# Kernel optimization log

Measured on AMD Instinct MI355X. Metric: run time of the kernel, lower is better.

The kernel has to match this reference:

```python
import jax, jax.numpy as jnp
import numpy as np

BS, DIM, EMB_DIM, SRC, TDEC, NEMB = 64, 512, 512, 400, 100, 50257


def intra_attention(h_t, h, W_attn):
    # h_t: [bs, dim]; h: [n, bs, dim]; W_attn: [dim, dim]
    n, bs, dim = h.shape
    # Faithful to torch .view([bs, dim, n]) on a contiguous [n, bs, dim]
    # tensor: raw row-major memory reinterpretation (NOT a transpose).
    hv = jnp.reshape(h, (bs, dim, n))  # [bs, dim, n]
    # E_t = (h_t @ W) [bs,1,dim] bmm hv [bs,dim,n] -> [bs, n]
    E = jnp.einsum('bd,bdn->bn', h_t @ W_attn, hv)
    # sum-normalized (non-softmax) score, eq. (4)
    A = E / jnp.sum(E, axis=1, keepdims=True)  # [bs, n]
    C = jnp.einsum('bdn,bn->bd', hv, A)        # [bs, dim]
    return A, C


def pointer_generator(ae_t, ce_t, hd_t, cd_t, W_emb, W_proj, W_u, b_u, b_out):
    # c_cat: [3*dim, bs]
    c_cat = jnp.concatenate((hd_t, ce_t, cd_t), axis=1).T
    # p_switch: [bs]
    p_switch = jax.nn.sigmoid(W_u @ c_cat + b_u).squeeze(0)
    # shared-embedding output projection, sect 2.4
    W_out = jnp.tanh(W_emb @ W_proj)           # [n_emb, 3*dim]
    logits = W_out @ c_cat + b_out             # [n_emb, bs]
    p_vocab = jax.nn.softmax(logits, axis=0)   # softmax over vocab
    p_gen = ((1.0 - p_switch) * p_vocab).T     # [bs, n_emb]
    p_copy = p_switch[:, None] * ae_t          # [bs, src]
    return p_gen, p_copy


def setup_inputs() -> dict:
    key = jax.random.key(0)
    ks = jax.random.split(key, 12)
    inp = {
        'h_t': jax.random.uniform(ks[0], (BS, DIM), dtype=jnp.float32),
        'h_enc': jax.random.uniform(ks[1], (SRC, BS, DIM), dtype=jnp.float32),
        'h_dec': jax.random.uniform(ks[2], (TDEC, BS, DIM), dtype=jnp.float32),
        'x': jax.random.randint(ks[3], (SRC, BS, 1), 0, NEMB, dtype=jnp.int64) if jax.config.jax_enable_x64 else jax.random.randint(ks[3], (SRC, BS, 1), 0, NEMB, dtype=jnp.int32),
        # positive attention weights keep the sum-normalized score well-conditioned
        'W_attn_enc': jax.random.uniform(ks[4], (DIM, DIM), dtype=jnp.float32, maxval=0.05),
        'W_attn_dec': jax.random.uniform(ks[5], (DIM, DIM), dtype=jnp.float32, maxval=0.05),
        'W_emb': jax.random.normal(ks[6], (NEMB, EMB_DIM), dtype=jnp.float32) * 0.02,
        'W_proj': jax.random.normal(ks[7], (EMB_DIM, 3 * DIM), dtype=jnp.float32) * 0.02,
        'W_u': jax.random.normal(ks[8], (1, 3 * DIM), dtype=jnp.float32) * 0.02,
        'b_u': jnp.zeros((1,), dtype=jnp.float32),
        'b_out': jnp.zeros((NEMB, 1), dtype=jnp.float32),
    }
    return inp


def reference(h_t, h_enc, h_dec, x, W_attn_enc, W_attn_dec, W_emb, W_proj, W_u, b_u, b_out):
    # one decode step of ReinforcedDecoder: enc attn + dec attn + pointer-gen
    ae_t, ce_t = intra_attention(h_t, h_enc, W_attn_enc)
    ad_t, cd_t = intra_attention(h_t, h_dec, W_attn_dec)
    p_gen, p_copy = pointer_generator(ae_t, ce_t, h_t, cd_t,
                                      W_emb, W_proj, W_u, b_u, b_out)
    return p_gen, p_copy
```

## Files before the change

### kernel.cpp

```cpp
#include <hip/hip_runtime.h>
#include <math.h>

typedef __attribute__((ext_vector_type(8))) short bf16x8;
typedef __attribute__((ext_vector_type(4))) float f32x4;
typedef __attribute__((ext_vector_type(4))) float f4v;

#define BS   64
#define DIM  512
#define SRC  400
#define TDEC 100
#define NEMB 50257
#define K3   1536

#define WS_Q     0
#define WS_EENC  65536
#define WS_EDEC  91136
#define WS_CENC  97536
#define WS_CDEC  130304
#define WS_ESUM  163072
#define WS_PSW   163200
#define WS_SMAX  163264
#define WS_SSUM  163328
#define WS_WPT   163392
#define WS_CCB   556608
#define WS_ZBEG  WS_CENC
#define WS_ZCNT  (WS_WPT - WS_CENC)

__device__ __forceinline__ ushort f2bf(float x) {
    union { float f; unsigned u; } v; v.f = x;
    unsigned r = (v.u + 0x7FFFu + ((v.u >> 16) & 1u)) >> 16;
    return (ushort)r;
}
__device__ __forceinline__ bf16x8 pack8v(f4v a, f4v b) {
    union { ushort us[8]; bf16x8 v; } p;
    p.us[0] = f2bf(a.x); p.us[1] = f2bf(a.y); p.us[2] = f2bf(a.z); p.us[3] = f2bf(a.w);
    p.us[4] = f2bf(b.x); p.us[5] = f2bf(b.y); p.us[6] = f2bf(b.z); p.us[7] = f2bf(b.w);
    return p.v;
}
__device__ __forceinline__ float pade_tanh(float x) {
    const float x2 = x * x;
    const float num = x * fmaf(x2, 1.0f / 15.0f, 1.0f);
    const float den = fmaf(x2, 0.4f, 1.0f);
    return num * __frcp_rn(den);
}
__device__ __forceinline__ void gl2lds16(const void* g, void* l) {
    __builtin_amdgcn_global_load_lds(
        (const __attribute__((address_space(1))) unsigned int*)g,
        (__attribute__((address_space(3))) unsigned int*)l, 16, 0, 0);
}

__global__ __launch_bounds__(256) void k_prep(const float* __restrict__ h_t,
                                              const float* __restrict__ Wenc,
                                              const float* __restrict__ Wdec,
                                              const float* __restrict__ Wp,
                                              float* __restrict__ ws) {
    __shared__ float sh[128 * 68];
    const int tid = threadIdx.x;
    if (blockIdx.x < 32) {
        const int which = blockIdx.x >> 4;
        const int c0 = (blockIdx.x & 15) * 32;
        const float* W = which ? Wdec : Wenc;
        float* q = ws + WS_Q + which * (BS * DIM);
        float* hS = sh;
        float* WSm = sh + 64 * 65;
        const int c = tid & 31, bg = tid >> 5;
        float acc[8] = {0.f, 0.f, 0.f, 0.f, 0.f, 0.f, 0.f, 0.f};
        for (int kc = 0; kc < 8; ++kc) {
            __syncthreads();
            #pragma unroll
            for (int r = 0; r < 16; ++r) {
                const int idx = r * 256 + tid;
                const int b = idx >> 6, k = idx & 63;
                hS[b * 65 + k] = h_t[b * DIM + kc * 64 + k];
            }
            #pragma unroll
            for (int r = 0; r < 8; ++r) {
                const int idx = r * 256 + tid;
                const int k = idx >> 5, cc = idx & 31;
                WSm[k * 33 + cc] = W[(size_t)(kc * 64 + k) * DIM + c0 + cc];
            }
            __syncthreads();
            #pragma unroll 8
            for (int k = 0; k < 64; ++k) {
                const float wv = WSm[k * 33 + c];
                #pragma unroll
                for (int bb = 0; bb < 8; ++bb)
                    acc[bb] = fmaf(hS[(bg * 8 + bb) * 65 + k], wv, acc[bb]);
            }
        }
        #pragma unroll
        for (int bb = 0; bb < 8; ++bb)
            q[(bg * 8 + bb) * DIM + c0 + c] = acc[bb];
    } else {
        const int bid = blockIdx.x - 32;
        const int t = bid >> 2, c = bid & 3;
        float (*T32)[68] = (float (*)[68])sh;
        #pragma unroll
        for (int p = 0; p < 8; ++p) {
            const int idx = p * 256 + tid;
            const int kk = idx >> 4, s = idx & 15;
            const float4 v = *(const float4*)(Wp + (size_t)(c * 128 + kk) * K3 + t * 64 + s * 4);
            T32[kk][s * 4 + 0] = v.x; T32[kk][s * 4 + 1] = v.y;
            T32[kk][s * 4 + 2] = v.z; T32[kk][s * 4 + 3] = v.w;
        }
        __syncthreads();
        char* dst = (char*)(ws + WS_WPT) + (size_t)bid * 16384;
        #pragma unroll
        for (int p = 0; p < 4; ++p) {
            const int fid = p * 256 + tid;
            const int lane = fid & 63;
            const int J = (fid >> 6) & 3;
            const int ks = fid >> 8;
            const int j = J * 16 + (lane & 15);
            const int k0 = ks * 32 + (lane >> 4) * 8;
            f4v a, b;
            a.x = T32[k0 + 0][j]; a.y = T32[k0 + 1][j];
            a.z = T32[k0 + 2][j]; a.w = T32[k0 + 3][j];
            b.x = T32[k0 + 4][j]; b.y = T32[k0 + 5][j];
            b.z = T32[k0 + 6][j]; b.w = T32[k0 + 7][j];
            *(bf16x8*)(dst + fid * 16) = pack8v(a, b);
        }
    }
}

#define IC 16
__global__ __launch_bounds__(256) void k_attn(const float* __restrict__ h_enc,
                                              const float* __restrict__ h_dec,
                                              float* __restrict__ ws) {
    const int b = blockIdx.x, which = blockIdx.y, z = blockIdx.z;
    const int tid = threadIdx.x;
    const int n   = which ? TDEC : SRC;
    const int per = which ? (TDEC / 4) : (SRC / 4);
    const int i_begin = z * per, i_end = i_begin + per;
    const float* h  = which ? h_dec : h_enc;
    const float* q  = ws + WS_Q + which * (BS * DIM) + b * DIM;
    float* wsE      = ws + (which ? WS_EDEC : WS_EENC) + b * n;
    float* Cws      = ws + (which ? WS_CDEC : WS_CENC) + b * DIM;
    const float* hb = h + (size_t)b * DIM * n;

    __shared__ float hS[DIM * (IC + 1)];
    __shared__ float qs[DIM];
    __shared__ float Ered[256];
    __shared__ float Es[IC];

    qs[tid] = q[tid];
    qs[tid + 256] = q[tid + 256];

    const int ii = tid & (IC - 1);
    const int dg = tid >> 4;
    float c0 = 0.f, c1 = 0.f, esum = 0.f;

    for (int i0 = i_begin; i0 < i_end; i0 += IC) {
        const int ic = min(IC, i_end - i0);
        __syncthreads();
        #pragma unroll 8
        for (int idx = tid; idx < DIM * IC; idx += 256) {
            const int d = idx >> 4, i = idx & (IC - 1);
            hS[d * (IC + 1) + i] = (i < ic) ? hb[(size_t)d * n + i0 + i] : 0.f;
        }
        __syncthreads();
        float p = 0.f;
        #pragma unroll 8
        for (int d = dg * 32; d < dg * 32 + 32; ++d) p += qs[d] * hS[d * (IC + 1) + ii];
        Ered[dg * IC + ii] = p;
        __syncthreads();
        if (tid < IC) {
            float e = 0.f;
            #pragma unroll
            for (int g = 0; g < 16; ++g) e += Ered[g * IC + tid];
            Es[tid] = e;
            esum += e;
            if (tid < ic) wsE[i0 + tid] = e;
        }
        __syncthreads();
        #pragma unroll
        for (int i = 0; i < IC; ++i) {
            const float e = Es[i];
            c0 += hS[tid * (IC + 1) + i] * e;
            c1 += hS[(tid + 256) * (IC + 1) + i] * e;
        }
    }
    atomicAdd(&Cws[tid], c0);
    atomicAdd(&Cws[tid + 256], c1);
    __syncthreads();
    if (tid < IC) Ered[tid] = esum;
    __syncthreads();
    if (tid == 0) {
        float s = 0.f;
        #pragma unroll
        for (int g = 0; g < IC; ++g) s += Ered[g];
        atomicAdd(&ws[WS_ESUM + which * 64 + b], s);
    }
}

__global__ void k_pswitch(const float* __restrict__ h_t,
                          const float* __restrict__ W_u,
                          const float* __restrict__ b_u,
                          float* __restrict__ out_copy,
                          float* __restrict__ ws) {
    const int b = blockIdx.x, tid = threadIdx.x;
    const float invE = 1.f / ws[WS_ESUM + b];
    const float invD = 1.f / ws[WS_ESUM + 64 + b];
    const float* Ce = ws + WS_CENC + b * DIM;
    const float* Cd = ws + WS_CDEC + b * DIM;
    ushort* ccB = (ushort*)(ws + WS_CCB);
    __shared__ float red[256];
    float part = 0.f;
    #pragma unroll
    for (int r = 0; r < 6; ++r) {
        const int j = tid + r * 256;
        float v = (j < DIM) ? h_t[b * DIM + j]
                            : ((j < 2 * DIM) ? Ce[j - DIM] * invE : Cd[j - 2 * DIM] * invD);
        ccB[(size_t)b * K3 + j] = f2bf(v);
        part += W_u[j] * v;
    }
    red[tid] = part;
    __syncthreads();
    for (int s = 128; s > 0; s >>= 1) {
        if (tid < s) red[tid] += red[tid + s];
        __syncthreads();
    }
    const float ps = 1.f / (1.f + expf(-(red[0] + b_u[0])));
    if (tid == 0) ws[WS_PSW + b] = ps;
    const float* Ee = ws + WS_EENC + b * SRC;
    for (int i = tid; i < SRC; i += 256) out_copy[b * SRC + i] = ps * Ee[i] * invE;
}

#define VB 128
#define WAITV(N) asm volatile("s_waitcnt vmcnt(" #N ")" ::: "memory")
__global__ __launch_bounds__(256, 2) void k_bigmm(const float* __restrict__ We,
                                                  const float* __restrict__ ws,
                                                  const float* __restrict__ b_out,
                                                  float* __restrict__ out) {
    __shared__ __align__(16) char smem[65536];
    const ushort* ccB = (const ushort*)(ws + WS_CCB);
    const char* wptb  = (const char*)(ws + WS_WPT);

    const int tid  = threadIdx.x;
    const int w    = tid >> 6, lane = tid & 63;
    const int lrow = lane & 15, lgrp = lane >> 4;
    const int vw   = blockIdx.x * VB + w * 32;
    const int row0 = vw + lrow, row1 = vw + 16 + lrow;
    char* tbase = smem + 49152 + w * 4096;
    const int swz = (lrow & 7) << 4;

    #pragma unroll
    for (int p = 0; p < 3; ++p) {
        const char* src = wptb + (size_t)p * 16384 + tid * 16;
        char* dst = smem + p * 16384 + tid * 16;
        #pragma unroll
        for (int rnd = 0; rnd < 4; ++rnd) gl2lds16(src + rnd * 4096, dst + rnd * 4096);
    }

    bf16x8 A0[16], A1[16];
    if (row0 < NEMB) {
        const f4v* p = (const f4v*)(We + (size_t)row0 * DIM + lgrp * 8);
        #pragma unroll
        for (int f = 0; f < 16; ++f)
            A0[f] = pack8v(__builtin_nontemporal_load(p + f * 8),
                           __builtin_nontemporal_load(p + f * 8 + 1));
    } else {
        #pragma unroll
        for (int f = 0; f < 16; ++f) A0[f] = (bf16x8){0, 0, 0, 0, 0, 0, 0, 0};
    }
    if (row1 < NEMB) {
        const f4v* p = (const f4v*)(We + (size_t)row1 * DIM + lgrp * 8);
        #pragma unroll
        for (int f = 0; f < 16; ++f)
            A1[f] = pack8v(__builtin_nontemporal_load(p + f * 8),
                           __builtin_nontemporal_load(p + f * 8 + 1));
    } else {
        #pragma unroll
        for (int f = 0; f < 16; ++f) A1[f] = (bf16x8){0, 0, 0, 0, 0, 0, 0, 0};
    }

    f32x4 La0[4], La1[4], Ta0[4], Ta1[4];
    #pragma unroll
    for (int i = 0; i < 4; ++i) {
        La0[i] = (f32x4){0.f, 0.f, 0.f, 0.f}; La1[i] = (f32x4){0.f, 0.f, 0.f, 0.f};
        Ta0[i] = (f32x4){0.f, 0.f, 0.f, 0.f}; Ta1[i] = (f32x4){0.f, 0.f, 0.f, 0.f};
    }

    for (int it = 0; it < 8; ++it) {
        #pragma unroll
        for (int u = 0; u < 12; ++u) {
            const int i = it * 12 + u;
            if (u == 10)      { if (it == 7) WAITV(4); else WAITV(8); }
            else if (u == 11) { if (it == 7) WAITV(0); else WAITV(8); }
            else              { WAITV(8); }
            __builtin_amdgcn_s_barrier();
            {
                const char* bp = smem + (u % 3) * 16384 + lane * 16;
                #pragma unroll
                for (int ks = 0; ks < 4; ++ks) {
                    const bf16x8 b0 = *(const bf16x8*)(bp + ks * 4096);
                    const bf16x8 b1 = *(const bf16x8*)(bp + ks * 4096 + 1024);
                    const bf16x8 b2 = *(const bf16x8*)(bp + ks * 4096 + 2048);
                    const bf16x8 b3 = *(const bf16x8*)(bp + ks * 4096 + 3072);
                    Ta0[0] = __builtin_amdgcn_mfma_f32_16x16x32_bf16(A0[(u & 3) * 4 + ks], b0, Ta0[0], 0, 0, 0);
                    Ta1[0] = __builtin_amdgcn_mfma_f32_16x16x32_bf16(A1[(u & 3) * 4 + ks], b0, Ta1[0], 0, 0, 0);
                    Ta0[1] = __builtin_amdgcn_mfma_f32_16x16x32_bf16(A0[(u & 3) * 4 + ks], b1, Ta0[1], 0, 0, 0);
                    Ta1[1] = __builtin_amdgcn_mfma_f32_16x16x32_bf16(A1[(u & 3) * 4 + ks], b1, Ta1[1], 0, 0, 0);
                    Ta0[2] = __builtin_amdgcn_mfma_f32_16x16x32_bf16(A0[(u & 3) * 4 + ks], b2, Ta0[2], 0, 0, 0);
                    Ta1[2] = __builtin_amdgcn_mfma_f32_16x16x32_bf16(A1[(u & 3) * 4 + ks], b2, Ta1[2], 0, 0, 0);
                    Ta0[3] = __builtin_amdgcn_mfma_f32_16x16x32_bf16(A0[(u & 3) * 4 + ks], b3, Ta0[3], 0, 0, 0);
                    Ta1[3] = __builtin_amdgcn_mfma_f32_16x16x32_bf16(A1[(u & 3) * 4 + ks], b3, Ta1[3], 0, 0, 0);
                }
            }
            if ((u & 3) == 3) {
                const int t = it * 3 + (u >> 2);
                #pragma unroll
                for (int nj = 0; nj < 4; ++nj) {
                    const int j = nj * 16 + lrow;
                    #pragma unroll
                    for (int r = 0; r < 4; ++r) {
                        const int v = lgrp * 4 + r;
                        *(ushort*)(tbase + v * 128 + ((j * 2) ^ ((v & 7) << 4))) =
                            f2bf(pade_tanh(Ta0[nj][r]));
                        *(ushort*)(tbase + (16 + v) * 128 + ((j * 2) ^ ((v & 7) << 4))) =
                            f2bf(pade_tanh(Ta1[nj][r]));
                    }
                }
                #pragma unroll
                for (int kc = 0; kc < 2; ++kc) {
                    const bf16x8 tf0 = *(const bf16x8*)(tbase + lrow * 128 +
                                                        ((kc * 64 + lgrp * 16) ^ swz));
                    const bf16x8 tf1 = *(const bf16x8*)(tbase + (16 + lrow) * 128 +
                                                        ((kc * 64 + lgrp * 16) ^ swz));
                    const ushort* cc = ccB + (size_t)lrow * K3 + t * 64 + kc * 32 + lgrp * 8;
                    const bf16x8 c0 = *(const bf16x8*)(cc);
                    const bf16x8 c1 = *(const bf16x8*)(cc + 16 * K3);
                    const bf16x8 c2 = *(const bf16x8*)(cc + 32 * K3);
                    const bf16x8 c3 = *(const bf16x8*)(cc + 48 * K3);
                    La0[0] = __builtin_amdgcn_mfma_f32_16x16x32_bf16(tf0, c0, La0[0], 0, 0, 0);
                    La1[0] = __builtin_amdgcn_mfma_f32_16x16x32_bf16(tf1, c0, La1[0], 0, 0, 0);
                    La0[1] = __builtin_amdgcn_mfma_f32_16x16x32_bf16(tf0, c1, La0[1], 0, 0, 0);
                    La1[1] = __builtin_amdgcn_mfma_f32_16x16x32_bf16(tf1, c1, La1[1], 0, 0, 0);
                    La0[2] = __builtin_amdgcn_mfma_f32_16x16x32_bf16(tf0, c2, La0[2], 0, 0, 0);
                    La1[2] = __builtin_amdgcn_mfma_f32_16x16x32_bf16(tf1, c2, La1[2], 0, 0, 0);
                    La0[3] = __builtin_amdgcn_mfma_f32_16x16x32_bf16(tf0, c3, La0[3], 0, 0, 0);
                    La1[3] = __builtin_amdgcn_mfma_f32_16x16x32_bf16(tf1, c3, La1[3], 0, 0, 0);
                }
                #pragma unroll
                for (int z = 0; z < 4; ++z) {
                    Ta0[z] = (f32x4){0.f, 0.f, 0.f, 0.f};
                    Ta1[z] = (f32x4){0.f, 0.f, 0.f, 0.f};
                }
            }
            __builtin_amdgcn_s_barrier();
            if (i + 3 < 96) {
                const char* src = wptb + (size_t)(i + 3) * 16384 + tid * 16;
                char* dst = smem + (u % 3) * 16384 + tid * 16;
                #pragma unroll
                for (int rnd = 0; rnd < 4; ++rnd)
                    gl2lds16(src + rnd * 4096, dst + rnd * 4096);
            }
        }
    }

    #pragma unroll
    for (int nb = 0; nb < 4; ++nb) {
        const int b = nb * 16 + lrow;
        #pragma unroll
        for (int r = 0; r < 4; ++r) {
            const int v0 = vw + lgrp * 4 + r;
            const int v1 = v0 + 16;
            if (v0 < NEMB) out[(size_t)b * NEMB + v0] = La0[nb][r] + b_out[v0];
            if (v1 < NEMB) out[(size_t)b * NEMB + v1] = La1[nb][r] + b_out[v1];
        }
    }
}

__global__ __launch_bounds__(1024) void k_softmax(float* __restrict__ out,
                                                  const float* __restrict__ ws) {
    const int b = blockIdx.x, tid = threadIdx.x;
    float* L = out + (size_t)b * NEMB;
    __shared__ float red[1024];
    float m = -1e30f;
    for (int v = tid; v < NEMB; v += 1024) m = fmaxf(m, L[v]);
    red[tid] = m;
    __syncthreads();
    for (int s = 512; s > 0; s >>= 1) {
        if (tid < s) red[tid] = fmaxf(red[tid], red[tid + s]);
        __syncthreads();
    }
    const float mb = red[0];
    __syncthreads();
    float sum = 0.f;
    for (int v = tid; v < NEMB; v += 1024) sum += expf(L[v] - mb);
    red[tid] = sum;
    __syncthreads();
    for (int s = 512; s > 0; s >>= 1) {
        if (tid < s) red[tid] += red[tid + s];
        __syncthreads();
    }
    const float scale = (1.f - ws[WS_PSW + b]) / red[0];
    for (int v = tid; v < NEMB; v += 1024) L[v] = expf(L[v] - mb) * scale;
}

extern "C" void kernel_launch(void* const* d_in, const int* in_sizes, int n_in,
                              void* d_out, int out_size, void* d_ws, size_t ws_size,
                              hipStream_t stream) {
    const float* h_t        = (const float*)d_in[0];
    const float* h_enc      = (const float*)d_in[1];
    const float* h_dec      = (const float*)d_in[2];
    const float* W_attn_enc = (const float*)d_in[4];
    const float* W_attn_dec = (const float*)d_in[5];
    const float* W_emb      = (const float*)d_in[6];
    const float* W_proj     = (const float*)d_in[7];
    const float* W_u        = (const float*)d_in[8];
    const float* b_u        = (const float*)d_in[9];
    const float* b_out      = (const float*)d_in[10];

    float* out = (float*)d_out;
    float* ws  = (float*)d_ws;
    float* out_copy = out + (size_t)BS * NEMB;

    hipMemsetAsync(ws + WS_ZBEG, 0, (size_t)WS_ZCNT * sizeof(float), stream);
    k_prep   <<<128, 256, 0, stream>>>(h_t, W_attn_enc, W_attn_dec, W_proj, ws);
    k_attn   <<<dim3(64, 2, 4), 256, 0, stream>>>(h_enc, h_dec, ws);
    k_pswitch<<<64, 256, 0, stream>>>(h_t, W_u, b_u, out_copy, ws);
    k_bigmm  <<<(NEMB + VB - 1) / VB, 256, 0, stream>>>(W_emb, ws, b_out, out);
    k_softmax<<<64, 1024, 0, stream>>>(out, ws);
}
```

Measured before the change: 339.0 us.

## Stage context in LDS, double-buffer Wproj, add setprio, split softmax across blocks

The concatenated context vector is now written pre-swizzled into an MFMA fragment layout and streamed into LDS per tile, replacing strided global loads inside the second GEMM. The Wproj pipeline drops from triple to double buffering, which frees LDS for the context tile, and the waitcnt schedule is adjusted to match. MFMA sections are wrapped in s_setprio. The 64-block softmax is replaced by a two-pass split: per-chunk max/sum statistics followed by a wider normalize kernel, to raise parallelism. The trade-off is an extra launch and a shallower prefetch depth.

```diff
diff --git a/kernel.cpp b/kernel.cpp
--- a/kernel.cpp
+++ b/kernel.cpp
@@ -20,9 +20,9 @@
 #define WS_ESUM  163072
 #define WS_PSW   163200
 #define WS_SMAX  163264
-#define WS_SSUM  163328
-#define WS_WPT   163392
-#define WS_CCB   556608
+#define WS_SSUM  163520
+#define WS_WPT   163776
+#define WS_CCF   556992
 #define WS_ZBEG  WS_CENC
 #define WS_ZCNT  (WS_WPT - WS_CENC)
 
@@ -203,15 +203,18 @@
     const float invD = 1.f / ws[WS_ESUM + 64 + b];
     const float* Ce = ws + WS_CENC + b * DIM;
     const float* Cd = ws + WS_CDEC + b * DIM;
-    ushort* ccB = (ushort*)(ws + WS_CCB);
+    ushort* ccF = (ushort*)(ws + WS_CCF);
     __shared__ float red[256];
+    const int nb = b >> 4, bl = b & 15;
     float part = 0.f;
     #pragma unroll
     for (int r = 0; r < 6; ++r) {
         const int j = tid + r * 256;
         float v = (j < DIM) ? h_t[b * DIM + j]
                             : ((j < 2 * DIM) ? Ce[j - DIM] * invE : Cd[j - 2 * DIM] * invD);
-        ccB[(size_t)b * K3 + j] = f2bf(v);
+        const int t = j >> 6, jj = j & 63;
+        const int kc = jj >> 5, lsub = (jj >> 3) & 3, e = jj & 7;
+        ccF[t * 4096 + kc * 2048 + nb * 512 + (lsub * 16 + bl) * 8 + e] = f2bf(v);
         part += W_u[j] * v;
     }
     red[tid] = part;
@@ -232,20 +235,21 @@
                                                   const float* __restrict__ ws,
                                                   const float* __restrict__ b_out,
                                                   float* __restrict__ out) {
-    __shared__ __align__(16) char smem[65536];
-    const ushort* ccB = (const ushort*)(ws + WS_CCB);
-    const char* wptb  = (const char*)(ws + WS_WPT);
+    __shared__ __align__(16) char smem[57344];
+    const char* wptb = (const char*)(ws + WS_WPT);
+    const char* ccfb = (const char*)(ws + WS_CCF);
 
     const int tid  = threadIdx.x;
     const int w    = tid >> 6, lane = tid & 63;
     const int lrow = lane & 15, lgrp = lane >> 4;
     const int vw   = blockIdx.x * VB + w * 32;
     const int row0 = vw + lrow, row1 = vw + 16 + lrow;
-    char* tbase = smem + 49152 + w * 4096;
+    char* ccL   = smem + 32768;
+    char* tbase = smem + 40960 + w * 4096;
     const int swz = (lrow & 7) << 4;
 
     #pragma unroll
-    for (int p = 0; p < 3; ++p) {
+    for (int p = 0; p < 2; ++p) {
         const char* src = wptb + (size_t)p * 16384 + tid * 16;
         char* dst = smem + p * 16384 + tid * 16;
         #pragma unroll
@@ -285,12 +289,13 @@
         #pragma unroll
         for (int u = 0; u < 12; ++u) {
             const int i = it * 12 + u;
-            if (u == 10)      { if (it == 7) WAITV(4); else WAITV(8); }
-            else if (u == 11) { if (it == 7) WAITV(0); else WAITV(8); }
-            else              { WAITV(8); }
+            if (u == 11)           { if (it == 7) { WAITV(0); } else { WAITV(4); } }
+            else if ((u & 3) == 1) { WAITV(6); }
+            else                   { WAITV(4); }
             __builtin_amdgcn_s_barrier();
             {
-                const char* bp = smem + (u % 3) * 16384 + lane * 16;
+                const char* bp = smem + (u & 1) * 16384 + lane * 16;
+                __builtin_amdgcn_s_setprio(1);
                 #pragma unroll
                 for (int ks = 0; ks < 4; ++ks) {
                     const bf16x8 b0 = *(const bf16x8*)(bp + ks * 4096);
@@ -306,9 +311,9 @@
                     Ta0[3] = __builtin_amdgcn_mfma_f32_16x16x32_bf16(A0[(u & 3) * 4 + ks], b3, Ta0[3], 0, 0, 0);
                     Ta1[3] = __builtin_amdgcn_mfma_f32_16x16x32_bf16(A1[(u & 3) * 4 + ks], b3, Ta1[3], 0, 0, 0);
                 }
+                __builtin_amdgcn_s_setprio(0);
             }
             if ((u & 3) == 3) {
-                const int t = it * 3 + (u >> 2);
                 #pragma unroll
                 for (int nj = 0; nj < 4; ++nj) {
                     const int j = nj * 16 + lrow;
@@ -321,17 +326,18 @@
                             f2bf(pade_tanh(Ta1[nj][r]));
                     }
                 }
+                __builtin_amdgcn_s_setprio(1);
                 #pragma unroll
                 for (int kc = 0; kc < 2; ++kc) {
                     const bf16x8 tf0 = *(const bf16x8*)(tbase + lrow * 128 +
                                                         ((kc * 64 + lgrp * 16) ^ swz));
                     const bf16x8 tf1 = *(const bf16x8*)(tbase + (16 + lrow) * 128 +
                                                         ((kc * 64 + lgrp * 16) ^ swz));
-                    const ushort* cc = ccB + (size_t)lrow * K3 + t * 64 + kc * 32 + lgrp * 8;
-                    const bf16x8 c0 = *(const bf16x8*)(cc);
-                    const bf16x8 c1 = *(const bf16x8*)(cc + 16 * K3);
-                    const bf16x8 c2 = *(const bf16x8*)(cc + 32 * K3);
-                    const bf16x8 c3 = *(const bf16x8*)(cc + 48 * K3);
+                    const char* cb = ccL + kc * 4096 + lane * 16;
+                    const bf16x8 c0 = *(const bf16x8*)(cb);
+                    const bf16x8 c1 = *(const bf16x8*)(cb + 1024);
+                    const bf16x8 c2 = *(const bf16x8*)(cb + 2048);
+                    const bf16x8 c3 = *(const bf16x8*)(cb + 3072);
                     La0[0] = __builtin_amdgcn_mfma_f32_16x16x32_bf16(tf0, c0, La0[0], 0, 0, 0);
                     La1[0] = __builtin_amdgcn_mfma_f32_16x16x32_bf16(tf1, c0, La1[0], 0, 0, 0);
                     La0[1] = __builtin_amdgcn_mfma_f32_16x16x32_bf16(tf0, c1, La0[1], 0, 0, 0);
@@ -341,6 +347,7 @@
                     La0[3] = __builtin_amdgcn_mfma_f32_16x16x32_bf16(tf0, c3, La0[3], 0, 0, 0);
                     La1[3] = __builtin_amdgcn_mfma_f32_16x16x32_bf16(tf1, c3, La1[3], 0, 0, 0);
                 }
+                __builtin_amdgcn_s_setprio(0);
                 #pragma unroll
                 for (int z = 0; z < 4; ++z) {
                     Ta0[z] = (f32x4){0.f, 0.f, 0.f, 0.f};
@@ -348,9 +355,16 @@
                 }
             }
             __builtin_amdgcn_s_barrier();
-            if (i + 3 < 96) {
-                const char* src = wptb + (size_t)(i + 3) * 16384 + tid * 16;
-                char* dst = smem + (u % 3) * 16384 + tid * 16;
+            if ((u & 3) == 0) {
+                const int t = it * 3 + (u >> 2);
+                const char* csrc = ccfb + (size_t)t * 8192 + tid * 16;
+                char* cdst = ccL + tid * 16;
+                gl2lds16(csrc, cdst);
+                gl2lds16(csrc + 4096, cdst + 4096);
+            }
+            if (i + 2 < 96) {
+                const char* src = wptb + (size_t)(i + 2) * 16384 + tid * 16;
+                char* dst = smem + (u & 1) * 16384 + tid * 16;
                 #pragma unroll
                 for (int rnd = 0; rnd < 4; ++rnd)
                     gl2lds16(src + rnd * 4096, dst + rnd * 4096);
@@ -371,31 +385,50 @@
     }
 }
 
-__global__ __launch_bounds__(1024) void k_softmax(float* __restrict__ out,
-                                                  const float* __restrict__ ws) {
-    const int b = blockIdx.x, tid = threadIdx.x;
+#define VCC 12565
+__global__ void k_colstat(const float* __restrict__ out, float* __restrict__ ws) {
+    const int b = blockIdx.x, vc = blockIdx.y, tid = threadIdx.x;
+    const float* L = out + (size_t)b * NEMB;
+    const int v0 = vc * VCC, vend = min(v0 + VCC, NEMB);
+    __shared__ float red[256];
+    float m = -1e30f;
+    for (int v = v0 + tid; v < vend; v += 256) m = fmaxf(m, L[v]);
+    red[tid] = m;
+    __syncthreads();
+    for (int s = 128; s > 0; s >>= 1) {
+        if (tid < s) red[tid] = fmaxf(red[tid], red[tid + s]);
+        __syncthreads();
+    }
+    const float mb = red[0];
+    __syncthreads();
+    float sum = 0.f;
+    for (int v = v0 + tid; v < vend; v += 256) sum += expf(L[v] - mb);
+    red[tid] = sum;
+    __syncthreads();
+    for (int s = 128; s > 0; s >>= 1) {
+        if (tid < s) red[tid] += red[tid + s];
+        __syncthreads();
+    }
+    if (tid == 0) {
+        ws[WS_SMAX + b * 4 + vc] = mb;
+        ws[WS_SSUM + b * 4 + vc] = red[0];
+    }
+}
+
+__global__ __launch_bounds__(256) void k_final(float* __restrict__ out,
+                                               const float* __restrict__ ws) {
+    const int b = blockIdx.x, seg = blockIdx.y, tid = threadIdx.x;
+    float m = -1e30f;
+    #pragma unroll
+    for (int p = 0; p < 4; ++p) m = fmaxf(m, ws[WS_SMAX + b * 4 + p]);
+    float s = 0.f;
+    #pragma unroll
+    for (int p = 0; p < 4; ++p)
+        s += ws[WS_SSUM + b * 4 + p] * expf(ws[WS_SMAX + b * 4 + p] - m);
+    const float scale = (1.f - ws[WS_PSW + b]) / s;
     float* L = out + (size_t)b * NEMB;
-    __shared__ float red[1024];
-    float m = -1e30f;
-    for (int v = tid; v < NEMB; v += 1024) m = fmaxf(m, L[v]);
-    red[tid] = m;
-    __syncthreads();
-    for (int s = 512; s > 0; s >>= 1) {
-        if (tid < s) red[tid] = fmaxf(red[tid], red[tid + s]);
-        __syncthreads();
-    }
-    const float mb = red[0];
-    __syncthreads();
-    float sum = 0.f;
-    for (int v = tid; v < NEMB; v += 1024) sum += expf(L[v] - mb);
-    red[tid] = sum;
-    __syncthreads();
-    for (int s = 512; s > 0; s >>= 1) {
-        if (tid < s) red[tid] += red[tid + s];
-        __syncthreads();
-    }
-    const float scale = (1.f - ws[WS_PSW + b]) / red[0];
-    for (int v = tid; v < NEMB; v += 1024) L[v] = expf(L[v] - mb) * scale;
+    const int v0 = seg * 3142, vend = min(v0 + 3142, NEMB);
+    for (int v = v0 + tid; v < vend; v += 256) L[v] = expf(L[v] - m) * scale;
 }
 
 extern "C" void kernel_launch(void* const* d_in, const int* in_sizes, int n_in,
@@ -421,5 +454,6 @@
     k_attn   <<<dim3(64, 2, 4), 256, 0, stream>>>(h_enc, h_dec, ws);
     k_pswitch<<<64, 256, 0, stream>>>(h_t, W_u, b_u, out_copy, ws);
     k_bigmm  <<<(NEMB + VB - 1) / VB, 256, 0, stream>>>(W_emb, ws, b_out, out);
-    k_softmax<<<64, 1024, 0, stream>>>(out, ws);
-}
+    k_colstat<<<dim3(64, 4), 256, 0, stream>>>(out, ws);
+    k_final  <<<dim3(64, 16), 256, 0, stream>>>(out, ws);
+}
```

Result: faster. 306.4 us (-9.6%).
